# Kernel optimization log

Measured on AMD Instinct MI355X. Metric: run time of the kernel, lower is better.

## Reference

```python
import jax, jax.numpy as jnp
import numpy as np

ROI = (8, 8)          # local window (kh, kw)
H = 768
W = 768
C = ROI[0] * ROI[1]   # 64 channels == prod(roi), required by the local conv
N_LAYERS = 4          # n_decoder_layers
LN_EPS = 1e-6         # flax.linen.LayerNorm default


def setup_inputs() -> dict:
    key = jax.random.key(0)
    k0, k1, k2 = jax.random.split(key, 3)
    x = jax.random.normal(k0, (H, W, C), jnp.float32)  # post-FPN feature map
    Ws = jax.random.normal(k1, (N_LAYERS, C, C), jnp.float32) / np.float32(np.sqrt(C))
    bs = jnp.zeros((N_LAYERS, C), jnp.float32)
    ln_scale = jnp.ones((N_LAYERS, C), jnp.float32)
    ln_bias = jnp.zeros((N_LAYERS, C), jnp.float32)
    w_out = jax.random.normal(k2, (C, 1), jnp.float32) / np.float32(np.sqrt(C))
    b_out = jnp.zeros((1,), jnp.float32)
    return {"x": x, "Ws": Ws, "bs": bs, "ln_scale": ln_scale,
            "ln_bias": ln_bias, "w_out": w_out, "b_out": b_out}


def att(x, weights):
    # out[i,j,c] = sum_{di,dj} xpad[i+di, j+dj, c] * weights[i, j, di*kw+dj]
    # Equivalent to the original per-channel lax.scan over
    # conv_general_dilated_local (window ordering row-major, 'same' padding),
    # but batched over all C channels at once via shifted-slice accumulation
    # instead of materializing the (H, W, 64, C) patch tensor.
    kh, kw = ROI
    pt, pb = (kh - 1) // 2, kh - 1 - (kh - 1) // 2  # 'SAME' pad for even kernel: (3, 4)
    pl, pr = (kw - 1) // 2, kw - 1 - (kw - 1) // 2
    xpad = jnp.pad(x, ((pt, pb), (pl, pr), (0, 0)))

    def body(acc, k):
        di = k // kw
        dj = k % kw
        patch = jax.lax.dynamic_slice(xpad, (di, dj, 0), (H, W, C))
        return acc + patch * weights[:, :, k][:, :, None], None

    acc, _ = jax.lax.scan(body, jnp.zeros_like(x), jnp.arange(kh * kw))
    return acc


def layer_norm(x, scale, bias):
    mu = jnp.mean(x, axis=-1, keepdims=True)
    var = jnp.mean(jnp.square(x - mu), axis=-1, keepdims=True)
    return (x - mu) * jax.lax.rsqrt(var + LN_EPS) * scale + bias


def reference(x, Ws, bs, ln_scale, ln_bias, w_out, b_out):
    weights = jax.nn.sigmoid(x)            # spatially-varying local-conv weights
    x0 = att(x, weights)                   # (H, W, C)
    for i in range(N_LAYERS):              # MLP decoder stack
        x0 = jax.nn.relu(x0 @ Ws[i] + bs[i])
        x0 = layer_norm(x0, ln_scale[i], ln_bias[i])
    out = x0 @ w_out + b_out               # (H, W, 1)
    return (x0, out)
```

## Files before the change

kernel.cpp:

```cpp
#include <hip/hip_runtime.h>
#include <hip/hip_bf16.h>


#define HH 768
#define WW 768
#define HWPX (HH*WW)

typedef __attribute__((ext_vector_type(8))) short short8;
typedef __attribute__((ext_vector_type(8))) _Float16 half8;
typedef __attribute__((ext_vector_type(4))) float f32x4;
typedef __attribute__((ext_vector_type(16))) float f32x16;

union hcvt { _Float16 h; ushort u; };
__device__ __forceinline__ ushort f2h(float f) { hcvt c; c.h = (_Float16)f; return c.u; }
__device__ __forceinline__ float sigmoidf(float v) { return 1.f / (1.f + __expf(-v)); }

__device__ __forceinline__ int goff(int row, int g) {
  return (row << 8) + (((g & ~7) | ((g ^ row) & 7)) << 3);
}
__device__ __forceinline__ int eoff(int row, int k) {
  const int g = k >> 3;
  return (row << 8) + (((g & ~7) | ((g ^ row) & 7)) << 3) + (k & 7);
}

__global__ __launch_bounds__(256)
void prep_wf(const float* __restrict__ Ws, const float* __restrict__ bs,
             const float* __restrict__ lns, const float* __restrict__ lnb,
             ushort* __restrict__ Wfg) {
  const int L = threadIdx.x >> 6, co = threadIdx.x & 63;
  float bias = bs[L * 64 + co];
  float colsum = 0.f;
  ushort* row = Wfg + (size_t)(L * 64 + co) * 80;
  for (int ci = 0; ci < 64; ++ci) {
    const float w = Ws[((L * 64 + ci) << 6) + co];
    const float sc = (L > 0) ? lns[(L - 1) * 64 + ci] : 1.f;
    const float wp = sc * w;
    if (L > 0) bias += lnb[(L - 1) * 64 + ci] * w;
    colsum += wp;
    row[ci] = f2h(wp);
  }
  row[64] = f2h(bias);
  row[65] = f2h(colsum);
  for (int q = 66; q < 80; ++q) row[q] = 0;
}

template<bool F16OUT>
__global__ __launch_bounds__(256, 2)
void att_k1(const float* __restrict__ x, void* __restrict__ attout) {
  __shared__ __align__(16) ushort Mb[64 * 256];
  __shared__ __align__(16) ushort Xb[64 * 256];
  const int tid = threadIdx.x;
  const int lane = tid & 63, w = tid >> 6;
  const int l15 = lane & 15, lg = lane >> 4;
  const int l31 = lane & 31, lh = lane >> 5;

  {
    const short8 z8 = {0,0,0,0,0,0,0,0};
    #pragma unroll
    for (int i = 0; i < 8; ++i)
      *reinterpret_cast<short8*>(&Mb[(tid + i * 256) * 8]) = z8;
  }

  const int b = blockIdx.x;
  const int tbase = (b & 7) * 1152 + (b >> 3) * 18;
  const int p  = w * 16 + l15;
  const int pr = p >> 3, pc = p & 7;
  const int cb = lg << 4;
  const int pb = w >> 1, cb2 = w & 1;

  float4 cv[4];
  float Rv[4][8];
  float Lv[4][8];
  short8 rs[4];

  auto issue_loads = [&](int ti, int tj, bool fresh) {
    {
      const float* cp = x + ((size_t)((ti + pr) * WW + (tj + pc)) << 6) + cb;
      #pragma unroll
      for (int qd = 0; qd < 4; ++qd)
        cv[qd] = *reinterpret_cast<const float4*>(cp + qd * 4);
    }
    #pragma unroll
    for (int i = 0; i < 4; ++i) {
      const int r = w + 4 * i;
      if (r < 15) {
        const int gr = min(max(ti + r - 3, 0), HH - 1);
        const float* rowp = x + ((size_t)gr * WW << 6) + lane;
        #pragma unroll
        for (int s = 0; s < 8; ++s) {
          const int gc = min(max(tj + 5 + s, 0), WW - 1);
          Rv[i][s] = rowp[(size_t)gc << 6];
        }
        if (fresh) {
          #pragma unroll
          for (int s = 0; s < 8; ++s) {
            const int gc = min(max(tj - 3 + s, 0), WW - 1);
            Lv[i][s] = rowp[(size_t)gc << 6];
          }
        }
      }
    }
  };

  auto write_lds = [&](int ti, int tj, bool fresh) {
    #pragma unroll
    for (int qd = 0; qd < 4; ++qd) {
      const float vs[4] = {cv[qd].x, cv[qd].y, cv[qd].z, cv[qd].w};
      #pragma unroll
      for (int j = 0; j < 4; ++j) {
        const int ch = cb + qd * 4 + j;
        const int k = ((pr + (ch >> 3)) << 4) | (pc + (ch & 7));
        Mb[eoff(p, k)] = f2h(sigmoidf(vs[j]));
      }
    }
    #pragma unroll
    for (int i = 0; i < 4; ++i) {
      const int r = w + 4 * i;
      if (r < 15) {
        const int gr = ti + r - 3;
        const bool rok = (unsigned)gr < (unsigned)HH;
        short8 left8;
        if (fresh) {
          #pragma unroll
          for (int s = 0; s < 8; ++s) {
            const int j = tj - 3 + s;
            const bool ok = rok && ((unsigned)j < (unsigned)WW);
            left8[s] = (short)f2h(ok ? Lv[i][s] : 0.f);
          }
        } else {
          left8 = rs[i];
        }
        short8 right8;
        #pragma unroll
        for (int s = 0; s < 8; ++s) {
          const int j = tj + 5 + s;
          const bool ok = rok && ((unsigned)j < (unsigned)WW);
          right8[s] = (short)f2h(ok ? Rv[i][s] : 0.f);
        }
        *reinterpret_cast<short8*>(&Xb[goff(lane, 2 * r)])     = left8;
        *reinterpret_cast<short8*>(&Xb[goff(lane, 2 * r + 1)]) = right8;
        rs[i] = right8;
      }
    }
  };

  f32x16 acc0, acc1;
  int pti = 0, ptj = 0;

  auto store_acc = [&](int ti, int tj) {
    #pragma unroll
    for (int reg = 0; reg < 16; ++reg) {
      const float v = acc0[reg] + acc1[reg];
      const int prow = (reg & 3) + 8 * (reg >> 2) + 4 * lh;
      const int p2 = pb * 32 + prow;
      const size_t gpx = (size_t)(ti + (p2 >> 3)) * WW + (tj + (p2 & 7));
      const int ch = cb2 * 32 + l31;
      if (F16OUT) ((ushort*)attout)[(gpx << 6) + ch] = f2h(v);
      else        ((float*)attout)[(gpx << 6) + ch] = v;
    }
  };

  issue_loads((tbase / 96) * 8, (tbase % 96) * 8, true);

  for (int t18 = 0; t18 < 18; ++t18) {
    const int tile = tbase + t18;
    const int ti = (tile / 96) * 8, tj = (tile % 96) * 8;
    const bool fresh = (t18 == 0) || (tj == 0);

    __syncthreads();
    write_lds(ti, tj, fresh);
    __syncthreads();

    if (t18 > 0) store_acc(pti, ptj);
    if (t18 < 17) {
      const int nt = tile + 1;
      issue_loads((nt / 96) * 8, (nt % 96) * 8, (nt % 96) == 0);
    }

    acc0 = (f32x16){0,0,0,0,0,0,0,0,0,0,0,0,0,0,0,0};
    acc1 = (f32x16){0,0,0,0,0,0,0,0,0,0,0,0,0,0,0,0};
    #pragma unroll
    for (int ks = 0; ks < 15; ++ks) {
      const int g = 2 * ks + lh;
      const half8 a  = *reinterpret_cast<const half8*>(&Mb[goff(pb * 32 + l31, g)]);
      const half8 bb = *reinterpret_cast<const half8*>(&Xb[goff(cb2 * 32 + l31, g)]);
      if (ks & 1) acc1 = __builtin_amdgcn_mfma_f32_32x32x16_f16(a, bb, acc1, 0, 0, 0);
      else        acc0 = __builtin_amdgcn_mfma_f32_32x32x16_f16(a, bb, acc0, 0, 0, 0);
    }
    pti = ti; ptj = tj;
  }
  store_acc(pti, ptj);
}

__device__ __forceinline__ float zsel(const f32x16& z0, const f32x16& z1, int nb, int idx) {
  return nb ? z1[idx] : z0[idx];
}

template<bool F16IN>
__global__ __launch_bounds__(512, 2)
void mlp_k2(const void* attv, const ushort* __restrict__ Wfg,
            const float* __restrict__ lns, const float* __restrict__ lnb,
            const float* __restrict__ w_out, const float* __restrict__ b_out,
            float* x0_out, float* __restrict__ out1) {
  __shared__ __align__(16) ushort wt[4 * 64 * 88];
  __shared__ __align__(16) ushort act[8][32 * 88];
  __shared__ __align__(16) ushort kpat[16];
  const int tid = threadIdx.x;
  const int lane = tid & 63, wid = tid >> 6;
  const int l31 = lane & 31, lh = lane >> 5;

  for (int idx = tid; idx < 4 * 64 * 10; idx += 512) {
    const int row = idx / 10, q = idx - row * 10;
    *reinterpret_cast<uint4*>(&wt[row * 88 + q * 8]) =
        *reinterpret_cast<const uint4*>(&Wfg[(size_t)row * 80 + q * 8]);
  }
  for (int idx = tid; idx < 256; idx += 512) {
    ushort* rp = &act[idx >> 5][(idx & 31) * 88];
    for (int q = 64; q < 88; ++q) rp[q] = 0;
    rp[64] = 0x3C00;
  }
  if (tid < 16) kpat[tid] = (tid == 0) ? (ushort)0x3C00 : (ushort)0;

  float sc3[2][4][4], lb3[2][4][4], wo3[2][4][4];
  #pragma unroll
  for (int nb = 0; nb < 2; ++nb)
    #pragma unroll
    for (int hi = 0; hi < 4; ++hi)
      #pragma unroll
      for (int j = 0; j < 4; ++j) {
        const int ch = nb * 32 + hi * 8 + lh * 4 + j;
        sc3[nb][hi][j] = lns[192 + ch];
        lb3[nb][hi][j] = lnb[192 + ch];
        wo3[nb][hi][j] = w_out[ch];
      }
  const float b0s = b_out[0];
  __syncthreads();

  ushort* const myact = act[wid];

  for (int it = 0; it < 9; ++it) {
    const int px = ((it * 256 + (int)blockIdx.x) * 8 + wid) * 32 + l31;

    half8 bfr[5];
    if (F16IN) {
      const ushort* ap = (const ushort*)attv + ((size_t)px << 6) + lh * 8;
      #pragma unroll
      for (int g = 0; g < 4; ++g)
        bfr[g] = *reinterpret_cast<const half8*>(ap + g * 16);
    } else {
      const float* ap = (const float*)attv + ((size_t)px << 6) + lh * 8;
      #pragma unroll
      for (int g = 0; g < 4; ++g) {
        const float4 fa = *reinterpret_cast<const float4*>(ap + g * 16);
        const float4 fb = *reinterpret_cast<const float4*>(ap + g * 16 + 4);
        half8 h;
        h[0]=(_Float16)fa.x; h[1]=(_Float16)fa.y; h[2]=(_Float16)fa.z; h[3]=(_Float16)fa.w;
        h[4]=(_Float16)fb.x; h[5]=(_Float16)fb.y; h[6]=(_Float16)fb.z; h[7]=(_Float16)fb.w;
        bfr[g] = h;
      }
    }
    bfr[4] = *reinterpret_cast<const half8*>(&kpat[lh * 8]);

    f32x16 z0, z1;
    float mu = 0.f, rstd = 1.f;
    #pragma unroll
    for (int L = 0; L < 4; ++L) {
      if (L > 0) {
        #pragma unroll
        for (int g = 0; g < 5; ++g)
          bfr[g] = *reinterpret_cast<const half8*>(&myact[l31 * 88 + g * 16 + lh * 8]);
      }
      z0 = (f32x16){0,0,0,0,0,0,0,0,0,0,0,0,0,0,0,0};
      z1 = (f32x16){0,0,0,0,0,0,0,0,0,0,0,0,0,0,0,0};
      #pragma unroll
      for (int g = 0; g < 5; ++g) {
        const half8 a0 = *reinterpret_cast<const half8*>(&wt[(L * 64      + l31) * 88 + g * 16 + lh * 8]);
        const half8 a1 = *reinterpret_cast<const half8*>(&wt[(L * 64 + 32 + l31) * 88 + g * 16 + lh * 8]);
        z0 = __builtin_amdgcn_mfma_f32_32x32x16_f16(a0, bfr[g], z0, 0, 0, 0);
        z1 = __builtin_amdgcn_mfma_f32_32x32x16_f16(a1, bfr[g], z1, 0, 0, 0);
      }
      float sp[4] = {0.f, 0.f, 0.f, 0.f}, qp[4] = {0.f, 0.f, 0.f, 0.f};
      #pragma unroll
      for (int r = 0; r < 16; ++r) {
        const float v0 = fmaxf(z0[r], 0.f); z0[r] = v0;
        const float v1 = fmaxf(z1[r], 0.f); z1[r] = v1;
        sp[r & 3] += v0 + v1;
        qp[r & 3] += v0 * v0 + v1 * v1;
      }
      float s = (sp[0] + sp[1]) + (sp[2] + sp[3]);
      float qq = (qp[0] + qp[1]) + (qp[2] + qp[3]);
      s  += __shfl_xor(s, 32, 64);
      qq += __shfl_xor(qq, 32, 64);
      mu = s * 0.015625f;
      const float var = qq * 0.015625f - mu * mu;
      rstd = rsqrtf(var + 1e-6f);
      if (L < 3) {
        #pragma unroll
        for (int nb = 0; nb < 2; ++nb)
          #pragma unroll
          for (int hi = 0; hi < 4; ++hi) {
            ushort4 pk;
            pk.x = f2h(rstd * zsel(z0, z1, nb, hi * 4 + 0));
            pk.y = f2h(rstd * zsel(z0, z1, nb, hi * 4 + 1));
            pk.z = f2h(rstd * zsel(z0, z1, nb, hi * 4 + 2));
            pk.w = f2h(rstd * zsel(z0, z1, nb, hi * 4 + 3));
            *reinterpret_cast<ushort4*>(&myact[l31 * 88 + nb * 32 + hi * 8 + lh * 4]) = pk;
          }
        if (lh == 0) myact[l31 * 88 + 65] = f2h(-(mu * rstd));
      }
    }

    const float t = mu * rstd;
    float part0 = 0.f, part1 = 0.f;
    #pragma unroll
    for (int nb = 0; nb < 2; ++nb)
      #pragma unroll
      for (int hi = 0; hi < 4; ++hi) {
        f32x4 yv;
        #pragma unroll
        for (int j = 0; j < 4; ++j) {
          const float v = zsel(z0, z1, nb, hi * 4 + j);
          const float y = v * (rstd * sc3[nb][hi][j]) + (lb3[nb][hi][j] - t * sc3[nb][hi][j]);
          yv[j] = y;
          if (j & 1) part1 += y * wo3[nb][hi][j];
          else       part0 += y * wo3[nb][hi][j];
        }
        *reinterpret_cast<f32x4*>(&x0_out[((size_t)px << 6) + nb * 32 + hi * 8 + lh * 4]) = yv;
      }
    float part = part0 + part1;
    part += __shfl_xor(part, 32, 64);
    if (lh == 0) out1[px] = part + b0s;
  }
}

extern "C" void kernel_launch(void* const* d_in, const int* in_sizes, int n_in,
                              void* d_out, int out_size, void* d_ws, size_t ws_size,
                              hipStream_t stream) {
  const float* x     = (const float*)d_in[0];
  const float* Ws    = (const float*)d_in[1];
  const float* bs    = (const float*)d_in[2];
  const float* lns   = (const float*)d_in[3];
  const float* lnbv  = (const float*)d_in[4];
  const float* w_out = (const float*)d_in[5];
  const float* b_out = (const float*)d_in[6];
  float* x0_out = (float*)d_out;
  float* out1   = x0_out + (size_t)HWPX * 64;

  const size_t attBytes = (size_t)HWPX * 64 * sizeof(ushort);
  if (ws_size >= attBytes + 65536) {
    ushort* atth = (ushort*)d_ws;
    ushort* Wfg  = (ushort*)((char*)d_ws + attBytes);
    prep_wf<<<1, 256, 0, stream>>>(Ws, bs, lns, lnbv, Wfg);
    att_k1<true><<<512, 256, 0, stream>>>(x, atth);
    mlp_k2<true><<<256, 512, 0, stream>>>(atth, Wfg, lns, lnbv,
                                          w_out, b_out, x0_out, out1);
  } else {
    ushort* Wfg = (ushort*)d_ws;
    prep_wf<<<1, 256, 0, stream>>>(Ws, bs, lns, lnbv, Wfg);
    att_k1<false><<<512, 256, 0, stream>>>(x, d_out);
    mlp_k2<false><<<256, 512, 0, stream>>>(d_out, Wfg, lns, lnbv,
                                           w_out, b_out, x0_out, out1);
  }
}
```

Baseline: 187.7 us.

## Split att_k1 K-reduction across two wave groups with LDS partial-sum exchange

```diff
diff --git a/kernel.cpp b/kernel.cpp
--- a/kernel.cpp
+++ b/kernel.cpp
@@ -45,44 +45,47 @@
 }
 
 template<bool F16OUT>
-__global__ __launch_bounds__(256, 2)
+__global__ __launch_bounds__(512, 4)
 void att_k1(const float* __restrict__ x, void* __restrict__ attout) {
   __shared__ __align__(16) ushort Mb[64 * 256];
   __shared__ __align__(16) ushort Xb[64 * 256];
+  __shared__ __align__(16) float  scr[4 * 4 * 64 * 4];
   const int tid = threadIdx.x;
   const int lane = tid & 63, w = tid >> 6;
   const int l15 = lane & 15, lg = lane >> 4;
   const int l31 = lane & 31, lh = lane >> 5;
+  const int ot = w & 3;
+  const int pb = ot >> 1, cb2 = ot & 1;
+  const int kh = w >> 2;
 
   {
     const short8 z8 = {0,0,0,0,0,0,0,0};
     #pragma unroll
-    for (int i = 0; i < 8; ++i)
-      *reinterpret_cast<short8*>(&Mb[(tid + i * 256) * 8]) = z8;
+    for (int i = 0; i < 4; ++i)
+      *reinterpret_cast<short8*>(&Mb[(tid + i * 512) * 8]) = z8;
   }
 
   const int b = blockIdx.x;
   const int tbase = (b & 7) * 1152 + (b >> 3) * 18;
-  const int p  = w * 16 + l15;
+  const int p  = (w & 3) * 16 + l15;
   const int pr = p >> 3, pc = p & 7;
-  const int cb = lg << 4;
-  const int pb = w >> 1, cb2 = w & 1;
-
-  float4 cv[4];
-  float Rv[4][8];
-  float Lv[4][8];
-  short8 rs[4];
+  const int cb = ((kh << 2) + lg) << 3;
+  const int kr0 = pr + (cb >> 3);
+
+  float4 cv[2];
+  float Rv[2][8];
+  float Lv[2][8];
+  short8 rs[2];
 
   auto issue_loads = [&](int ti, int tj, bool fresh) {
     {
       const float* cp = x + ((size_t)((ti + pr) * WW + (tj + pc)) << 6) + cb;
-      #pragma unroll
-      for (int qd = 0; qd < 4; ++qd)
-        cv[qd] = *reinterpret_cast<const float4*>(cp + qd * 4);
-    }
-    #pragma unroll
-    for (int i = 0; i < 4; ++i) {
-      const int r = w + 4 * i;
+      cv[0] = *reinterpret_cast<const float4*>(cp);
+      cv[1] = *reinterpret_cast<const float4*>(cp + 4);
+    }
+    #pragma unroll
+    for (int i = 0; i < 2; ++i) {
+      const int r = w + 8 * i;
       if (r < 15) {
         const int gr = min(max(ti + r - 3, 0), HH - 1);
         const float* rowp = x + ((size_t)gr * WW << 6) + lane;
@@ -104,18 +107,17 @@
 
   auto write_lds = [&](int ti, int tj, bool fresh) {
     #pragma unroll
-    for (int qd = 0; qd < 4; ++qd) {
+    for (int qd = 0; qd < 2; ++qd) {
       const float vs[4] = {cv[qd].x, cv[qd].y, cv[qd].z, cv[qd].w};
       #pragma unroll
       for (int j = 0; j < 4; ++j) {
-        const int ch = cb + qd * 4 + j;
-        const int k = ((pr + (ch >> 3)) << 4) | (pc + (ch & 7));
+        const int k = (kr0 << 4) + pc + qd * 4 + j;
         Mb[eoff(p, k)] = f2h(sigmoidf(vs[j]));
       }
     }
     #pragma unroll
-    for (int i = 0; i < 4; ++i) {
-      const int r = w + 4 * i;
+    for (int i = 0; i < 2; ++i) {
+      const int r = w + 8 * i;
       if (r < 15) {
         const int gr = ti + r - 3;
         const bool rok = (unsigned)gr < (unsigned)HH;
@@ -144,13 +146,13 @@
     }
   };
 
-  f32x16 acc0, acc1;
+  f32x16 acc;
   int pti = 0, ptj = 0;
 
   auto store_acc = [&](int ti, int tj) {
     #pragma unroll
     for (int reg = 0; reg < 16; ++reg) {
-      const float v = acc0[reg] + acc1[reg];
+      const float v = acc[reg];
       const int prow = (reg & 3) + 8 * (reg >> 2) + 4 * lh;
       const int p2 = pb * 32 + prow;
       const size_t gpx = (size_t)(ti + (p2 >> 3)) * WW + (tj + (p2 & 7));
@@ -168,28 +170,52 @@
     const bool fresh = (t18 == 0) || (tj == 0);
 
     __syncthreads();
+    if (kh == 0 && t18 > 0) {
+      #pragma unroll
+      for (int q = 0; q < 4; ++q) {
+        const float4 pv = *reinterpret_cast<const float4*>(&scr[ot * 1024 + q * 256 + lane * 4]);
+        acc[q * 4 + 0] += pv.x; acc[q * 4 + 1] += pv.y;
+        acc[q * 4 + 2] += pv.z; acc[q * 4 + 3] += pv.w;
+      }
+    }
     write_lds(ti, tj, fresh);
     __syncthreads();
-
-    if (t18 > 0) store_acc(pti, ptj);
+    if (kh == 0 && t18 > 0) store_acc(pti, ptj);
     if (t18 < 17) {
       const int nt = tile + 1;
       issue_loads((nt / 96) * 8, (nt % 96) * 8, (nt % 96) == 0);
     }
 
-    acc0 = (f32x16){0,0,0,0,0,0,0,0,0,0,0,0,0,0,0,0};
-    acc1 = (f32x16){0,0,0,0,0,0,0,0,0,0,0,0,0,0,0,0};
-    #pragma unroll
-    for (int ks = 0; ks < 15; ++ks) {
+    acc = (f32x16){0,0,0,0,0,0,0,0,0,0,0,0,0,0,0,0};
+    const int ks0 = kh ? 7 : 0, ks1 = kh ? 15 : 7;
+    #pragma unroll 8
+    for (int ks = ks0; ks < ks1; ++ks) {
       const int g = 2 * ks + lh;
       const half8 a  = *reinterpret_cast<const half8*>(&Mb[goff(pb * 32 + l31, g)]);
       const half8 bb = *reinterpret_cast<const half8*>(&Xb[goff(cb2 * 32 + l31, g)]);
-      if (ks & 1) acc1 = __builtin_amdgcn_mfma_f32_32x32x16_f16(a, bb, acc1, 0, 0, 0);
-      else        acc0 = __builtin_amdgcn_mfma_f32_32x32x16_f16(a, bb, acc0, 0, 0, 0);
+      acc = __builtin_amdgcn_mfma_f32_32x32x16_f16(a, bb, acc, 0, 0, 0);
+    }
+    if (kh == 1) {
+      #pragma unroll
+      for (int q = 0; q < 4; ++q) {
+        float4 pv;
+        pv.x = acc[q * 4 + 0]; pv.y = acc[q * 4 + 1];
+        pv.z = acc[q * 4 + 2]; pv.w = acc[q * 4 + 3];
+        *reinterpret_cast<float4*>(&scr[ot * 1024 + q * 256 + lane * 4]) = pv;
+      }
     }
     pti = ti; ptj = tj;
   }
-  store_acc(pti, ptj);
+  __syncthreads();
+  if (kh == 0) {
+    #pragma unroll
+    for (int q = 0; q < 4; ++q) {
+      const float4 pv = *reinterpret_cast<const float4*>(&scr[ot * 1024 + q * 256 + lane * 4]);
+      acc[q * 4 + 0] += pv.x; acc[q * 4 + 1] += pv.y;
+      acc[q * 4 + 2] += pv.z; acc[q * 4 + 3] += pv.w;
+    }
+    store_acc(pti, ptj);
+  }
 }
 
 __device__ __forceinline__ float zsel(const f32x16& z0, const f32x16& z1, int nb, int idx) {
@@ -351,13 +377,13 @@
     ushort* atth = (ushort*)d_ws;
     ushort* Wfg  = (ushort*)((char*)d_ws + attBytes);
     prep_wf<<<1, 256, 0, stream>>>(Ws, bs, lns, lnbv, Wfg);
-    att_k1<true><<<512, 256, 0, stream>>>(x, atth);
+    att_k1<true><<<512, 512, 0, stream>>>(x, atth);
     mlp_k2<true><<<256, 512, 0, stream>>>(atth, Wfg, lns, lnbv,
                                           w_out, b_out, x0_out, out1);
   } else {
     ushort* Wfg = (ushort*)d_ws;
     prep_wf<<<1, 256, 0, stream>>>(Ws, bs, lns, lnbv, Wfg);
-    att_k1<false><<<512, 256, 0, stream>>>(x, d_out);
+    att_k1<false><<<512, 512, 0, stream>>>(x, d_out);
     mlp_k2<false><<<256, 512, 0, stream>>>(d_out, Wfg, lns, lnbv,
                                            w_out, b_out, x0_out, out1);
   }
```

After: 179.6 us. -4.3%, faster.
